# Kernel tuning notes

Hardware: AMD Instinct MI355X
Metric: run time of the kernel (lower is better)

## Reference

```python
import jax, jax.numpy as jnp
import numpy as np

K = 3          # s_kernel_size = max_graph_distance + 1
C_OUT = 128    # out_channel


def setup_inputs() -> dict:
    key = jax.random.key(0)
    k1, k2, k3, k4 = jax.random.split(key, 4)
    N, C_IN, T, V = 64, 64, 256, 25
    x = jax.random.normal(k1, (N, C_IN, T, V), dtype=jnp.float32)
    # 1x1 Conv2d(in_channel, out_channel*K) weight/bias
    W = jax.random.normal(k2, (K * C_OUT, C_IN), dtype=jnp.float32) * 0.05
    b = jax.random.normal(k3, (K * C_OUT,), dtype=jnp.float32) * 0.05
    # fixed adjacency stack (non-trainable buffer-like param)
    A = jax.random.uniform(k4, (K, V, V), dtype=jnp.float32)
    edge = jnp.ones((K, V, V), dtype=jnp.float32)       # init ones_like(A)
    adaptive_A = jnp.zeros((K, V, V), dtype=jnp.float32)  # init zeros_like(A)
    return {"x": x, "W": W, "b": b, "A": A, "edge": edge, "adaptive_A": adaptive_A}


def reference(x, W, b, A, edge, adaptive_A):
    n, c_in, t, v = x.shape
    # 1x1 conv == per-pixel GEMM over channel dim: (n,c,t,v) -> (n, K*C_OUT, t, v)
    y = jnp.einsum('nctv,oc->notv', x, W) + b[None, :, None, None]
    y = y.reshape(n, K, C_OUT, t, v)                 # (n, k, c, t, v)
    effective_A = A * edge + adaptive_A              # (k, v, w)
    out = jnp.einsum('nkctv,kvw->nctw', y, effective_A)
    return out
```

## Files before the change

kernel.cpp:

```cpp
#include <hip/hip_runtime.h>
#include <hip/hip_bf16.h>

typedef __bf16 bf16x8 __attribute__((ext_vector_type(8)));
typedef __bf16 bf16x4 __attribute__((ext_vector_type(4)));
typedef float floatx4 __attribute__((ext_vector_type(4)));
typedef float floatx4u __attribute__((ext_vector_type(4), aligned(4)));

#define ROWK 200
#define ZROWS 112

__global__ void sgc_prep(const float* __restrict__ W, const float* __restrict__ b,
                         const float* __restrict__ A, const float* __restrict__ edge,
                         const float* __restrict__ adA,
                         __hip_bfloat16* __restrict__ Wp, __hip_bfloat16* __restrict__ effAB,
                         float* __restrict__ bias2) {
  int tid = blockIdx.x * blockDim.x + threadIdx.x;
  int nthr = gridDim.x * blockDim.x;
  for (int i = tid; i < 24576; i += nthr) {
    int c = i / 192; int r = i - c * 192; int k = r >> 6; int ci = r & 63;
    Wp[i] = __float2bfloat16(W[(k * 128 + c) * 64 + ci]);
  }
  for (int i = tid; i < 2560; i += nthr) {
    int n = i >> 5; int v = i & 31;
    float val = 0.f;
    if (n < 75 && v < 25) {
      int k = n / 25; int w = n - k * 25;
      int idx = (k * 25 + v) * 25 + w;
      val = A[idx] * edge[idx] + adA[idx];
    }
    effAB[i] = __float2bfloat16(val);
  }
  for (int i = tid; i < 3200; i += nthr) {
    int c = i / 25; int w = i - c * 25;
    float s = 0.f;
    for (int k = 0; k < 3; k++) {
      float sv = 0.f;
      for (int v = 0; v < 25; v++) {
        int idx = (k * 25 + v) * 25 + w;
        sv += A[idx] * edge[idx] + adA[idx];
      }
      s += b[k * 128 + c] * sv;
    }
    bias2[i] = s;
  }
}

__global__ __launch_bounds__(256, 3)
void sgc_main(const float* __restrict__ x,
              const __hip_bfloat16* __restrict__ Wp,
              const __hip_bfloat16* __restrict__ effAB,
              const float* __restrict__ bias2,
              float* __restrict__ out) {
  __shared__ __hip_bfloat16 zt[ZROWS * ROWK];
  const int tid = threadIdx.x;
  const int lane = tid & 63;
  const int wv = tid >> 6;
  const int blk = blockIdx.x;

  const int col = lane & 15;
  const int quad = lane >> 4;
  const int kb = quad * 8;

  bf16x8 bA[5];
#pragma unroll
  for (int nt = 0; nt < 5; nt++)
    bA[nt] = *(const bf16x8*)(effAB + (nt * 16 + col) * 32 + kb);

  {
    const int g = blk * 4 + wv;
    const int n0 = g >> 8, t = g & 255;
    const float* xbase = x + (size_t)(n0 * 64) * 6400 + (size_t)t * 25;
#pragma unroll
    for (int mt = 0; mt < 4; mt++) {
      const int ci = mt * 16 + col;
      const float* xr = xbase + (size_t)ci * 6400;
      bf16x8 xa;
      if (quad < 3) {
        floatx4u a = *(const floatx4u*)(xr + kb);
        floatx4u c = *(const floatx4u*)(xr + kb + 4);
        xa = (bf16x8){(__bf16)a.x, (__bf16)a.y, (__bf16)a.z, (__bf16)a.w,
                      (__bf16)c.x, (__bf16)c.y, (__bf16)c.z, (__bf16)c.w};
      } else {
        float v24 = xr[24];
        xa = (bf16x8){(__bf16)v24, (__bf16)0.f, (__bf16)0.f, (__bf16)0.f,
                      (__bf16)0.f, (__bf16)0.f, (__bf16)0.f, (__bf16)0.f};
      }
      floatx4 zacc[5];
#pragma unroll
      for (int nt = 0; nt < 5; nt++) {
        zacc[nt] = (floatx4){0.f, 0.f, 0.f, 0.f};
        zacc[nt] = __builtin_amdgcn_mfma_f32_16x16x32_bf16(xa, bA[nt], zacc[nt], 0, 0, 0);
      }
#pragma unroll
      for (int nt = 0; nt < 5; nt++) {
        int nn = nt * 16 + col;
        if (nn < 75) {
          int k = (nn * 41) >> 10;
          int w = nn - k * 25;
          bf16x4 zb = (bf16x4){(__bf16)zacc[nt][0], (__bf16)zacc[nt][1],
                               (__bf16)zacc[nt][2], (__bf16)zacc[nt][3]};
          *(bf16x4*)(zt + (wv * 25 + w) * ROWK + k * 64 + mt * 16 + quad * 4) = zb;
        }
      }
    }
  }

  bf16x8 afr[2][6];
#pragma unroll
  for (int mtl = 0; mtl < 2; mtl++) {
    int c = (2 * wv + mtl) * 16 + col;
    const __hip_bfloat16* wrow = Wp + c * 192;
#pragma unroll
    for (int ks = 0; ks < 6; ks++)
      afr[mtl][ks] = *(const bf16x8*)(wrow + ks * 32 + kb);
  }

  floatx4 acc[2][7];
#pragma unroll
  for (int nt = 0; nt < 7; nt++) {
    int nn = nt * 16 + col;
    int p = (nn * 41) >> 10;
    int w = nn - p * 25;
#pragma unroll
    for (int mtl = 0; mtl < 2; mtl++) {
      int c0 = (2 * wv + mtl) * 16 + quad * 4;
#pragma unroll
      for (int r = 0; r < 4; r++)
        acc[mtl][nt][r] = bias2[(c0 + r) * 25 + w];
    }
  }

  __syncthreads();

  const __hip_bfloat16* ztp = zt;
#pragma unroll
  for (int ks = 0; ks < 6; ks++) {
    bf16x8 bfr[7];
#pragma unroll
    for (int nt = 0; nt < 7; nt++)
      bfr[nt] = *(const bf16x8*)(ztp + (nt * 16 + col) * ROWK + ks * 32 + kb);
#pragma unroll
    for (int nt = 0; nt < 7; nt++) {
      acc[0][nt] = __builtin_amdgcn_mfma_f32_16x16x32_bf16(afr[0][ks], bfr[nt], acc[0][nt], 0, 0, 0);
      acc[1][nt] = __builtin_amdgcn_mfma_f32_16x16x32_bf16(afr[1][ks], bfr[nt], acc[1][nt], 0, 0, 0);
    }
  }

#pragma unroll
  for (int nt = 0; nt < 7; nt++) {
    int nn = nt * 16 + col;
    if (nn >= 100) continue;
    int p = (nn * 41) >> 10;
    int w = nn - p * 25;
    int g = blk * 4 + p;
    int n = g >> 8, t = g & 255;
#pragma unroll
    for (int mtl = 0; mtl < 2; mtl++) {
      int c0 = (2 * wv + mtl) * 16 + quad * 4;
      size_t base = ((size_t)(n * 128 + c0) * 256 + t) * 25 + w;
#pragma unroll
      for (int r = 0; r < 4; r++)
        out[base + (size_t)r * 6400] = acc[mtl][nt][r];
    }
  }
}

extern "C" void kernel_launch(void* const* d_in, const int* in_sizes, int n_in,
                              void* d_out, int out_size, void* d_ws, size_t ws_size,
                              hipStream_t stream) {
  const float* x    = (const float*)d_in[0];
  const float* W    = (const float*)d_in[1];
  const float* b    = (const float*)d_in[2];
  const float* A    = (const float*)d_in[3];
  const float* edge = (const float*)d_in[4];
  const float* adA  = (const float*)d_in[5];
  float* out = (float*)d_out;

  char* ws = (char*)d_ws;
  __hip_bfloat16* Wp    = (__hip_bfloat16*)ws;
  __hip_bfloat16* effAB = (__hip_bfloat16*)(ws + 49152);
  float* bias2          = (float*)(ws + 54272);

  sgc_prep<<<64, 256, 0, stream>>>(W, b, A, edge, adA, Wp, effAB, bias2);
  sgc_main<<<4096, 256, 0, stream>>>(x, Wp, effAB, bias2, out);
}
```

Measured before the change: 380.5 us.

## Split fused kernel into separate Z-compute and output GEMM kernels via global workspace

Replaces the single fused kernel, which staged the adjacency-mixed intermediate in shared memory, with two kernels. The first writes the bf16 intermediate z to a global workspace. The second runs the channel GEMM with 512-thread blocks over flat pixel-vertex columns. This drops the 44KB shared-memory allocation and the block barrier, which should allow higher occupancy. In exchange it adds a global round trip of z (about 63MB of bf16 written and read) plus an extra launch, and the output stores become less contiguous.

```diff
diff --git a/kernel.cpp b/kernel.cpp
--- a/kernel.cpp
+++ b/kernel.cpp
@@ -5,9 +5,6 @@
 typedef __bf16 bf16x4 __attribute__((ext_vector_type(4)));
 typedef float floatx4 __attribute__((ext_vector_type(4)));
 typedef float floatx4u __attribute__((ext_vector_type(4), aligned(4)));
-
-#define ROWK 200
-#define ZROWS 112
 
 __global__ void sgc_prep(const float* __restrict__ W, const float* __restrict__ b,
                          const float* __restrict__ A, const float* __restrict__ edge,
@@ -45,18 +42,13 @@
   }
 }
 
-__global__ __launch_bounds__(256, 3)
-void sgc_main(const float* __restrict__ x,
-              const __hip_bfloat16* __restrict__ Wp,
-              const __hip_bfloat16* __restrict__ effAB,
-              const float* __restrict__ bias2,
-              float* __restrict__ out) {
-  __shared__ __hip_bfloat16 zt[ZROWS * ROWK];
+__global__ __launch_bounds__(256, 4)
+void sgc_z(const float* __restrict__ x,
+           const __hip_bfloat16* __restrict__ effAB,
+           __hip_bfloat16* __restrict__ z) {
   const int tid = threadIdx.x;
   const int lane = tid & 63;
   const int wv = tid >> 6;
-  const int blk = blockIdx.x;
-
   const int col = lane & 15;
   const int quad = lane >> 4;
   const int kb = quad * 8;
@@ -66,102 +58,100 @@
   for (int nt = 0; nt < 5; nt++)
     bA[nt] = *(const bf16x8*)(effAB + (nt * 16 + col) * 32 + kb);
 
-  {
-    const int g = blk * 4 + wv;
-    const int n0 = g >> 8, t = g & 255;
-    const float* xbase = x + (size_t)(n0 * 64) * 6400 + (size_t)t * 25;
+  const int g = blockIdx.x * 4 + wv;
+  const int n0 = g >> 8, t = g & 255;
+  const float* xbase = x + (size_t)(n0 * 64) * 6400 + (size_t)t * 25;
+  __hip_bfloat16* zrow0 = z + (size_t)g * 25 * 192;
+
 #pragma unroll
-    for (int mt = 0; mt < 4; mt++) {
-      const int ci = mt * 16 + col;
-      const float* xr = xbase + (size_t)ci * 6400;
-      bf16x8 xa;
-      if (quad < 3) {
-        floatx4u a = *(const floatx4u*)(xr + kb);
-        floatx4u c = *(const floatx4u*)(xr + kb + 4);
-        xa = (bf16x8){(__bf16)a.x, (__bf16)a.y, (__bf16)a.z, (__bf16)a.w,
-                      (__bf16)c.x, (__bf16)c.y, (__bf16)c.z, (__bf16)c.w};
-      } else {
-        float v24 = xr[24];
-        xa = (bf16x8){(__bf16)v24, (__bf16)0.f, (__bf16)0.f, (__bf16)0.f,
-                      (__bf16)0.f, (__bf16)0.f, (__bf16)0.f, (__bf16)0.f};
-      }
-      floatx4 zacc[5];
+  for (int mt = 0; mt < 4; mt++) {
+    const int ci = mt * 16 + col;
+    const float* xr = xbase + (size_t)ci * 6400;
+    bf16x8 xa;
+    if (quad < 3) {
+      floatx4u a = *(const floatx4u*)(xr + kb);
+      floatx4u c = *(const floatx4u*)(xr + kb + 4);
+      xa = (bf16x8){(__bf16)a.x, (__bf16)a.y, (__bf16)a.z, (__bf16)a.w,
+                    (__bf16)c.x, (__bf16)c.y, (__bf16)c.z, (__bf16)c.w};
+    } else {
+      float v24 = xr[24];
+      xa = (bf16x8){(__bf16)v24, (__bf16)0.f, (__bf16)0.f, (__bf16)0.f,
+                    (__bf16)0.f, (__bf16)0.f, (__bf16)0.f, (__bf16)0.f};
+    }
+    floatx4 zacc[5];
 #pragma unroll
-      for (int nt = 0; nt < 5; nt++) {
-        zacc[nt] = (floatx4){0.f, 0.f, 0.f, 0.f};
-        zacc[nt] = __builtin_amdgcn_mfma_f32_16x16x32_bf16(xa, bA[nt], zacc[nt], 0, 0, 0);
-      }
+    for (int nt = 0; nt < 5; nt++) {
+      zacc[nt] = (floatx4){0.f, 0.f, 0.f, 0.f};
+      zacc[nt] = __builtin_amdgcn_mfma_f32_16x16x32_bf16(xa, bA[nt], zacc[nt], 0, 0, 0);
+    }
 #pragma unroll
-      for (int nt = 0; nt < 5; nt++) {
-        int nn = nt * 16 + col;
-        if (nn < 75) {
-          int k = (nn * 41) >> 10;
-          int w = nn - k * 25;
-          bf16x4 zb = (bf16x4){(__bf16)zacc[nt][0], (__bf16)zacc[nt][1],
-                               (__bf16)zacc[nt][2], (__bf16)zacc[nt][3]};
-          *(bf16x4*)(zt + (wv * 25 + w) * ROWK + k * 64 + mt * 16 + quad * 4) = zb;
-        }
+    for (int nt = 0; nt < 5; nt++) {
+      int nn = nt * 16 + col;
+      if (nn < 75) {
+        int k = (nn * 41) >> 10;
+        int w = nn - k * 25;
+        bf16x4 zb = (bf16x4){(__bf16)zacc[nt][0], (__bf16)zacc[nt][1],
+                             (__bf16)zacc[nt][2], (__bf16)zacc[nt][3]};
+        *(bf16x4*)(zrow0 + (size_t)w * 192 + k * 64 + mt * 16 + quad * 4) = zb;
       }
     }
   }
+}
 
-  bf16x8 afr[2][6];
-#pragma unroll
-  for (int mtl = 0; mtl < 2; mtl++) {
-    int c = (2 * wv + mtl) * 16 + col;
-    const __hip_bfloat16* wrow = Wp + c * 192;
+__global__ __launch_bounds__(512, 4)
+void sgc_out(const __hip_bfloat16* __restrict__ z,
+             const __hip_bfloat16* __restrict__ Wp,
+             const float* __restrict__ bias2,
+             float* __restrict__ out) {
+  const int tid = threadIdx.x;
+  const int lane = tid & 63;
+  const int wv = tid >> 6;
+  const int col = lane & 15;
+  const int quad = lane >> 4;
+  const int kb = quad * 8;
+  const int cg0 = blockIdx.x * 64;
+
+  bf16x8 afr[6];
+  {
+    const __hip_bfloat16* wrow = Wp + (wv * 16 + col) * 192;
 #pragma unroll
     for (int ks = 0; ks < 6; ks++)
-      afr[mtl][ks] = *(const bf16x8*)(wrow + ks * 32 + kb);
+      afr[ks] = *(const bf16x8*)(wrow + ks * 32 + kb);
   }
 
-  floatx4 acc[2][7];
+  floatx4 acc[4];
 #pragma unroll
-  for (int nt = 0; nt < 7; nt++) {
-    int nn = nt * 16 + col;
-    int p = (nn * 41) >> 10;
-    int w = nn - p * 25;
+  for (int nt = 0; nt < 4; nt++) {
+    int cg = cg0 + nt * 16 + col;
+    int w = cg % 25;
+    int c0 = wv * 16 + quad * 4;
 #pragma unroll
-    for (int mtl = 0; mtl < 2; mtl++) {
-      int c0 = (2 * wv + mtl) * 16 + quad * 4;
-#pragma unroll
-      for (int r = 0; r < 4; r++)
-        acc[mtl][nt][r] = bias2[(c0 + r) * 25 + w];
-    }
-  }
-
-  __syncthreads();
-
-  const __hip_bfloat16* ztp = zt;
-#pragma unroll
-  for (int ks = 0; ks < 6; ks++) {
-    bf16x8 bfr[7];
-#pragma unroll
-    for (int nt = 0; nt < 7; nt++)
-      bfr[nt] = *(const bf16x8*)(ztp + (nt * 16 + col) * ROWK + ks * 32 + kb);
-#pragma unroll
-    for (int nt = 0; nt < 7; nt++) {
-      acc[0][nt] = __builtin_amdgcn_mfma_f32_16x16x32_bf16(afr[0][ks], bfr[nt], acc[0][nt], 0, 0, 0);
-      acc[1][nt] = __builtin_amdgcn_mfma_f32_16x16x32_bf16(afr[1][ks], bfr[nt], acc[1][nt], 0, 0, 0);
-    }
+    for (int r = 0; r < 4; r++)
+      acc[nt][r] = bias2[(c0 + r) * 25 + w];
   }
 
 #pragma unroll
-  for (int nt = 0; nt < 7; nt++) {
-    int nn = nt * 16 + col;
-    if (nn >= 100) continue;
-    int p = (nn * 41) >> 10;
-    int w = nn - p * 25;
-    int g = blk * 4 + p;
-    int n = g >> 8, t = g & 255;
+  for (int ks = 0; ks < 6; ks++) {
+    bf16x8 bfr[4];
 #pragma unroll
-    for (int mtl = 0; mtl < 2; mtl++) {
-      int c0 = (2 * wv + mtl) * 16 + quad * 4;
-      size_t base = ((size_t)(n * 128 + c0) * 256 + t) * 25 + w;
+    for (int nt = 0; nt < 4; nt++)
+      bfr[nt] = *(const bf16x8*)(z + (size_t)(cg0 + nt * 16 + col) * 192 + ks * 32 + kb);
 #pragma unroll
-      for (int r = 0; r < 4; r++)
-        out[base + (size_t)r * 6400] = acc[mtl][nt][r];
-    }
+    for (int nt = 0; nt < 4; nt++)
+      acc[nt] = __builtin_amdgcn_mfma_f32_16x16x32_bf16(afr[ks], bfr[nt], acc[nt], 0, 0, 0);
+  }
+
+#pragma unroll
+  for (int nt = 0; nt < 4; nt++) {
+    int cg = cg0 + nt * 16 + col;
+    int pix = cg / 25;
+    int w = cg - pix * 25;
+    int n = pix >> 8, t = pix & 255;
+    int c0 = wv * 16 + quad * 4;
+    size_t base = ((size_t)(n * 128 + c0) * 256 + t) * 25 + w;
+#pragma unroll
+    for (int r = 0; r < 4; r++)
+      out[base + (size_t)r * 6400] = acc[nt][r];
   }
 }
 
@@ -180,7 +170,9 @@
   __hip_bfloat16* Wp    = (__hip_bfloat16*)ws;
   __hip_bfloat16* effAB = (__hip_bfloat16*)(ws + 49152);
   float* bias2          = (float*)(ws + 54272);
+  __hip_bfloat16* z     = (__hip_bfloat16*)(ws + 67584);
 
   sgc_prep<<<64, 256, 0, stream>>>(W, b, A, edge, adA, Wp, effAB, bias2);
-  sgc_main<<<4096, 256, 0, stream>>>(x, Wp, effAB, bias2, out);
+  sgc_z<<<4096, 256, 0, stream>>>(x, effAB, z);
+  sgc_out<<<6400, 512, 0, stream>>>(z, Wp, bias2, out);
 }
```

Measured after the change: 576.3 us. +51.4%, slower.
